# Kernel optimization log

Hardware: AMD Instinct MI355X
Metric: run time of the kernel (lower is better)

Reference implementation:

```python
import jax, jax.numpy as jnp
import numpy as np

N_NODES = 100000
N_EDGES = 1600000
IN_DIM = 128
HID = 64
CONV2_OUT = 8
GLOBAL_DIM = 24
OUT_DIM = 1
NUM_GRAPHS = 64
NEG_SLOPE = 0.01


def setup_inputs() -> dict:
    key = jax.random.key(0)
    ks = jax.random.split(key, 12)
    x = jax.random.normal(ks[0], (N_NODES, IN_DIM), dtype=jnp.float32)
    edge_index = jax.random.randint(ks[1], (2, N_EDGES), 0, N_NODES, dtype=jnp.int32)
    batch = jnp.sort(jax.random.randint(ks[2], (N_NODES,), 0, NUM_GRAPHS, dtype=jnp.int32))
    global_features = jax.random.normal(ks[3], (NUM_GRAPHS, GLOBAL_DIM), dtype=jnp.float32)
    # GCNConv weights (glorot-ish scale) and Linear weights
    W1 = jax.random.normal(ks[4], (IN_DIM, HID), dtype=jnp.float32) / np.sqrt(IN_DIM)
    b1 = jnp.zeros((HID,), dtype=jnp.float32)
    W2 = jax.random.normal(ks[5], (HID, CONV2_OUT), dtype=jnp.float32) / np.sqrt(HID)
    b2 = jnp.zeros((CONV2_OUT,), dtype=jnp.float32)
    fcW1 = jax.random.normal(ks[6], (GLOBAL_DIM + CONV2_OUT, 16), dtype=jnp.float32) / np.sqrt(GLOBAL_DIM + CONV2_OUT)
    fcb1 = jnp.zeros((16,), dtype=jnp.float32)
    fcW2 = jax.random.normal(ks[7], (16, OUT_DIM), dtype=jnp.float32) / np.sqrt(16)
    fcb2 = jnp.zeros((OUT_DIM,), dtype=jnp.float32)
    return {"x": x, "edge_index": edge_index, "batch": batch,
            "global_features": global_features,
            "W1": W1, "b1": b1, "W2": W2, "b2": b2,
            "fcW1": fcW1, "fcb1": fcb1, "fcW2": fcW2, "fcb2": fcb2}


def gcn_conv(x, src, dst, W, b):
    """PyG GCNConv: add self-loops, sym-normalize, aggregate x@W from src->dst."""
    n = x.shape[0]
    h = x @ W  # [N, F_out]
    loop = jnp.arange(n, dtype=src.dtype)
    src2 = jnp.concatenate([src, loop])
    dst2 = jnp.concatenate([dst, loop])
    deg = jax.ops.segment_sum(jnp.ones_like(dst2, dtype=h.dtype), dst2, num_segments=n)
    dinv = jnp.where(deg > 0, jax.lax.rsqrt(deg), 0.0)
    norm = dinv[src2] * dinv[dst2]  # [E+N]
    msg = h[src2] * norm[:, None]   # edge gather (dominant traffic)
    out = jax.ops.segment_sum(msg, dst2, num_segments=n)
    return out + b


def reference(x, edge_index, batch, global_features, W1, b1, W2, b2, fcW1, fcb1, fcW2, fcb2):
    src, dst = edge_index[0], edge_index[1]
    h = jax.nn.leaky_relu(gcn_conv(x, src, dst, W1, b1), NEG_SLOPE)
    h = jax.nn.leaky_relu(gcn_conv(h, src, dst, W2, b2), NEG_SLOPE)
    # global mean pool over graphs
    sums = jax.ops.segment_sum(h, batch, num_segments=NUM_GRAPHS)
    cnts = jax.ops.segment_sum(jnp.ones((h.shape[0],), h.dtype), batch, num_segments=NUM_GRAPHS)
    pool = sums / jnp.maximum(cnts, 1.0)[:, None]
    z = jnp.concatenate([pool, global_features], axis=1)
    z = jax.nn.leaky_relu(z @ fcW1 + fcb1, NEG_SLOPE)
    z = jax.nn.leaky_relu(z @ fcW2 + fcb2, NEG_SLOPE)
    return z
```

## Files before the change

### kernel.cpp

```cpp
#include <hip/hip_runtime.h>

constexpr int N_NODES = 100000;
constexpr int N_EDGES = 1600000;
constexpr int IN_DIM  = 128;
constexpr int HID     = 64;
constexpr int C2      = 8;
constexpr int GDIM    = 24;
constexpr int NG      = 64;
constexpr float SLOPE = 0.01f;
constexpr int NB_SCAN = (N_NODES + 255) / 256;

__device__ __forceinline__ float lrelu(float v) { return v > 0.f ? v : SLOPE * v; }

__device__ __forceinline__ float bflo(unsigned int u) { return __uint_as_float(u << 16); }
__device__ __forceinline__ float bfhi(unsigned int u) { return __uint_as_float(u & 0xffff0000u); }
__device__ __forceinline__ unsigned short f2bf(float f) {
    unsigned int i = __float_as_uint(f);
    unsigned int r = (i + 0x7fffu + ((i >> 16) & 1u)) >> 16;
    return (unsigned short)r;
}

__global__ void k_rank(const int* __restrict__ dst, int* __restrict__ deg,
                       int* __restrict__ rnk) {
    int t = blockIdx.x * 256 + threadIdx.x;
    if (t < N_EDGES / 4) {
        int4 d = ((const int4*)dst)[t];
        int4 r;
        r.x = atomicAdd(&deg[d.x], 1);
        r.y = atomicAdd(&deg[d.y], 1);
        r.z = atomicAdd(&deg[d.z], 1);
        r.w = atomicAdd(&deg[d.w], 1);
        ((int4*)rnk)[t] = r;
    }
}

__global__ void k_scan1(const int* __restrict__ deg, int* __restrict__ rowptr,
                        int* __restrict__ bsum, float* __restrict__ dinv) {
    __shared__ int s[256];
    int tid = threadIdx.x;
    int i = blockIdx.x * 256 + tid;
    int v = (i < N_NODES) ? deg[i] : 0;
    if (i < N_NODES) dinv[i] = rsqrtf((float)(v + 1));
    s[tid] = v;
    __syncthreads();
    for (int off = 1; off < 256; off <<= 1) {
        int t = (tid >= off) ? s[tid - off] : 0;
        __syncthreads();
        s[tid] += t;
        __syncthreads();
    }
    if (i < N_NODES) rowptr[i] = s[tid] - v;
    if (tid == 255) bsum[blockIdx.x] = s[255];
}

__global__ void k_scan2(const int* __restrict__ bsum, int* __restrict__ bsumx) {
    __shared__ int s[512];
    int tid = threadIdx.x;
    int v = (tid < NB_SCAN) ? bsum[tid] : 0;
    s[tid] = v;
    __syncthreads();
    for (int off = 1; off < 512; off <<= 1) {
        int t = (tid >= off) ? s[tid - off] : 0;
        __syncthreads();
        s[tid] += t;
        __syncthreads();
    }
    if (tid < NB_SCAN) bsumx[tid] = s[tid] - v;
}

__global__ void k_place(const int* __restrict__ src, const int* __restrict__ dst,
                        const int* __restrict__ rnk, const int* __restrict__ rowptr,
                        const int* __restrict__ bsumx, int* __restrict__ eidx) {
    int t = blockIdx.x * 256 + threadIdx.x;
    if (t < N_EDGES / 4) {
        int4 d = ((const int4*)dst)[t];
        int4 r = ((const int4*)rnk)[t];
        int4 s = ((const int4*)src)[t];
        int px = rowptr[d.x] + bsumx[d.x >> 8] + r.x;
        int py = rowptr[d.y] + bsumx[d.y >> 8] + r.y;
        int pz = rowptr[d.z] + bsumx[d.z >> 8] + r.z;
        int pw = rowptr[d.w] + bsumx[d.w >> 8] + r.w;
        eidx[px] = s.x; eidx[py] = s.y; eidx[pz] = s.z; eidx[pw] = s.w;
    }
}

__global__ __launch_bounds__(256) void k_gemm1(const float* __restrict__ x,
                                               const float* __restrict__ W1,
                                               const float* __restrict__ dinv,
                                               unsigned short* __restrict__ hs1) {
    __shared__ float sW[IN_DIM * HID];
    __shared__ float sX[32][IN_DIM];
    int node0 = blockIdx.x * 32;
    for (int t = threadIdx.x; t < IN_DIM * HID / 4; t += 256)
        ((float4*)sW)[t] = ((const float4*)W1)[t];
    for (int t = threadIdx.x; t < 32 * IN_DIM / 4; t += 256) {
        int r = t >> 5, c4 = t & 31;
        ((float4*)&sX[r][0])[c4] = ((const float4*)(x + (size_t)(node0 + r) * IN_DIM))[c4];
    }
    __syncthreads();
    int col = threadIdx.x & 63;
    int nb  = (threadIdx.x >> 6) * 8;
    float acc[8] = {0.f, 0.f, 0.f, 0.f, 0.f, 0.f, 0.f, 0.f};
    for (int k4 = 0; k4 < IN_DIM; k4 += 4) {
        float w0 = sW[(k4 + 0) * HID + col];
        float w1 = sW[(k4 + 1) * HID + col];
        float w2 = sW[(k4 + 2) * HID + col];
        float w3 = sW[(k4 + 3) * HID + col];
#pragma unroll
        for (int j = 0; j < 8; ++j) {
            float4 xv = *((const float4*)&sX[nb + j][k4]);
            acc[j] += xv.x * w0 + xv.y * w1 + xv.z * w2 + xv.w * w3;
        }
    }
#pragma unroll
    for (int j = 0; j < 8; ++j) {
        int n = node0 + nb + j;
        hs1[(size_t)n * HID + col] = f2bf(acc[j] * dinv[n]);
    }
}

__global__ __launch_bounds__(256) void k_agg1(const int* __restrict__ rowptr,
                                              const int* __restrict__ bsumx,
                                              const int* __restrict__ deg,
                                              const int* __restrict__ eidx,
                                              const unsigned short* __restrict__ hs1,
                                              const float* __restrict__ dinv,
                                              const float* __restrict__ b1,
                                              const float* __restrict__ W2,
                                              float* __restrict__ hs2) {
    int lane = threadIdx.x & 63;
    int q    = lane & 7;
    int slot = lane >> 3;
    float w2f[8];
#pragma unroll
    for (int i = 0; i < 8; ++i) w2f[i] = W2[(8 * q + i) * C2 + slot];
    float4 bb0 = ((const float4*)b1)[2 * q];
    float4 bb1 = ((const float4*)b1)[2 * q + 1];
    float bv[8] = {bb0.x, bb0.y, bb0.z, bb0.w, bb1.x, bb1.y, bb1.z, bb1.w};
    int node_base = blockIdx.x * 16 + (threadIdx.x >> 6) * 4;

    for (int nn = 0; nn < 4; ++nn) {
        int node  = node_base + nn;
        int start = rowptr[node] + bsumx[node >> 8];
        int cnt   = deg[node];
        uint4 hv = ((const uint4*)(hs1 + (size_t)node * HID))[q];
        float acc[8] = {0.f, 0.f, 0.f, 0.f, 0.f, 0.f, 0.f, 0.f};
        for (int base = 0; base < cnt; base += 64) {
            int idx = (base + lane < cnt) ? eidx[start + base + lane] : 0;
            int lim = min(64, cnt - base);
            int trips = (lim + 15) >> 4;
            for (int t = 0; t < trips; ++t) {
                int k0 = slot + t * 16;
                int k1 = k0 + 8;
                int s0 = __shfl(idx, k0);
                int s1 = __shfl(idx, k1 & 63);
                uint4 v0 = ((const uint4*)(hs1 + (size_t)s0 * HID))[q];
                uint4 v1 = ((const uint4*)(hs1 + (size_t)s1 * HID))[q];
                if (k0 >= lim) { v0.x = 0; v0.y = 0; v0.z = 0; v0.w = 0; }
                if (k1 >= lim) { v1.x = 0; v1.y = 0; v1.z = 0; v1.w = 0; }
                acc[0] += bflo(v0.x); acc[1] += bfhi(v0.x);
                acc[2] += bflo(v0.y); acc[3] += bfhi(v0.y);
                acc[4] += bflo(v0.z); acc[5] += bfhi(v0.z);
                acc[6] += bflo(v0.w); acc[7] += bfhi(v0.w);
                acc[0] += bflo(v1.x); acc[1] += bfhi(v1.x);
                acc[2] += bflo(v1.y); acc[3] += bfhi(v1.y);
                acc[4] += bflo(v1.z); acc[5] += bfhi(v1.z);
                acc[6] += bflo(v1.w); acc[7] += bfhi(v1.w);
            }
        }
#pragma unroll
        for (int m = 8; m < 64; m <<= 1)
#pragma unroll
            for (int i = 0; i < 8; ++i) acc[i] += __shfl_xor(acc[i], m);
        float self[8] = {bflo(hv.x), bfhi(hv.x), bflo(hv.y), bfhi(hv.y),
                         bflo(hv.z), bfhi(hv.z), bflo(hv.w), bfhi(hv.w)};
        float di = dinv[node];
        float p = 0.f;
#pragma unroll
        for (int i = 0; i < 8; ++i) {
            float y = lrelu(di * (acc[i] + self[i]) + bv[i]);
            p += y * w2f[i];
        }
#pragma unroll
        for (int m = 1; m < 8; m <<= 1) p += __shfl_xor(p, m);
        if (q == 0) hs2[(size_t)node * C2 + slot] = p * di;
    }
}

__global__ __launch_bounds__(256) void k_agg2(const int* __restrict__ rowptr,
                                              const int* __restrict__ bsumx,
                                              const int* __restrict__ deg,
                                              const int* __restrict__ eidx,
                                              const float* __restrict__ hs2,
                                              const float* __restrict__ dinv,
                                              const float* __restrict__ b2,
                                              float* __restrict__ y2) {
    int lane = threadIdx.x & 63;
    int q    = lane & 1;
    int slot = lane >> 1;
    int node_base = blockIdx.x * 16 + (threadIdx.x >> 6) * 4;

    for (int nn = 0; nn < 4; ++nn) {
        int node  = node_base + nn;
        int start = rowptr[node] + bsumx[node >> 8];
        int cnt   = deg[node];
        float4 acc = make_float4(0.f, 0.f, 0.f, 0.f);
        for (int base = 0; base < cnt; base += 64) {
            int idx = (base + lane < cnt) ? eidx[start + base + lane] : 0;
            int lim = min(64, cnt - base);
            int s0 = __shfl(idx, slot);
            int s1 = __shfl(idx, slot + 32);
            float4 v0 = ((const float4*)(hs2 + (size_t)s0 * C2))[q];
            float4 v1 = ((const float4*)(hs2 + (size_t)s1 * C2))[q];
            if (slot >= lim)      { v0.x = 0.f; v0.y = 0.f; v0.z = 0.f; v0.w = 0.f; }
            if (slot + 32 >= lim) { v1.x = 0.f; v1.y = 0.f; v1.z = 0.f; v1.w = 0.f; }
            acc.x += v0.x + v1.x; acc.y += v0.y + v1.y;
            acc.z += v0.z + v1.z; acc.w += v0.w + v1.w;
        }
        for (int m = 2; m < 64; m <<= 1) {
            acc.x += __shfl_xor(acc.x, m); acc.y += __shfl_xor(acc.y, m);
            acc.z += __shfl_xor(acc.z, m); acc.w += __shfl_xor(acc.w, m);
        }
        if (slot == 0) {
            float4 h = ((const float4*)(hs2 + (size_t)node * C2))[q];
            float di = dinv[node];
            const float* bb = b2 + q * 4;
            float4 r;
            r.x = lrelu(di * (acc.x + h.x) + bb[0]);
            r.y = lrelu(di * (acc.y + h.y) + bb[1]);
            r.z = lrelu(di * (acc.z + h.z) + bb[2]);
            r.w = lrelu(di * (acc.w + h.w) + bb[3]);
            ((float4*)(y2 + (size_t)node * C2))[q] = r;
        }
    }
}

__device__ __forceinline__ int lower_bound(const int* __restrict__ b, int n, int v) {
    int lo = 0, hi = n;
    while (lo < hi) {
        int m = (lo + hi) >> 1;
        if (b[m] < v) lo = m + 1; else hi = m;
    }
    return lo;
}

__global__ __launch_bounds__(256) void k_pool(const float* __restrict__ y2,
                                              const int* __restrict__ batch,
                                              const float* __restrict__ gfeat,
                                              const float* __restrict__ fcW1,
                                              const float* __restrict__ fcb1,
                                              const float* __restrict__ fcW2,
                                              const float* __restrict__ fcb2,
                                              float* __restrict__ out) {
    __shared__ float s[256];
    int g   = blockIdx.x;
    int tid = threadIdx.x;
    int start = lower_bound(batch, N_NODES, g);
    int end   = lower_bound(batch, N_NODES, g + 1);
    int col = tid & 7;
    float local = 0.f;
    for (int n = start + (tid >> 3); n < end; n += 32)
        local += y2[(size_t)n * C2 + col];
    s[tid] = local;
    __syncthreads();
    for (int off = 128; off >= 8; off >>= 1) {
        if (tid < off) s[tid] += s[tid + off];
        __syncthreads();
    }
    if (tid == 0) {
        float cnt = fmaxf((float)(end - start), 1.f);
        float z[C2 + GDIM];
        for (int c = 0; c < C2; ++c) z[c] = s[c] / cnt;
        for (int c = 0; c < GDIM; ++c) z[C2 + c] = gfeat[g * GDIM + c];
        float acc2 = fcb2[0];
        for (int j = 0; j < 16; ++j) {
            float acc = fcb1[j];
            for (int c = 0; c < C2 + GDIM; ++c) acc += z[c] * fcW1[c * 16 + j];
            acc2 += lrelu(acc) * fcW2[j];
        }
        out[g] = lrelu(acc2);
    }
}

extern "C" void kernel_launch(void* const* d_in, const int* in_sizes, int n_in,
                              void* d_out, int out_size, void* d_ws, size_t ws_size,
                              hipStream_t stream) {
    const float* x     = (const float*)d_in[0];
    const int*   ei    = (const int*)d_in[1];
    const int*   batch = (const int*)d_in[2];
    const float* gfeat = (const float*)d_in[3];
    const float* W1    = (const float*)d_in[4];
    const float* b1    = (const float*)d_in[5];
    const float* W2    = (const float*)d_in[6];
    const float* b2    = (const float*)d_in[7];
    const float* fcW1  = (const float*)d_in[8];
    const float* fcb1  = (const float*)d_in[9];
    const float* fcW2  = (const float*)d_in[10];
    const float* fcb2  = (const float*)d_in[11];
    const int* src = ei;
    const int* dst = ei + N_EDGES;

    char* ws = (char*)d_ws;
    size_t off = 0;
    auto alloc = [&](size_t bytes) -> void* {
        void* p = ws + off;
        off = (off + bytes + 255) & ~(size_t)255;
        return p;
    };
    int*   deg    = (int*)  alloc((size_t)N_NODES * 4);
    float* dinv   = (float*)alloc((size_t)N_NODES * 4);
    int*   rowptr = (int*)  alloc((size_t)N_NODES * 4);
    int*   bsum   = (int*)  alloc(512 * 4);
    int*   bsumx  = (int*)  alloc(512 * 4);
    int*   rnk    = (int*)  alloc((size_t)N_EDGES * 4);
    int*   eidx   = (int*)  alloc((size_t)N_EDGES * 4);
    unsigned short* hs1 = (unsigned short*)alloc((size_t)N_NODES * HID * 2);
    float* hs2    = (float*)alloc((size_t)N_NODES * C2 * 4);
    float* y2     = (float*)alloc((size_t)N_NODES * C2 * 4);

    hipMemsetAsync(deg, 0, (size_t)N_NODES * 4, stream);

    k_rank <<<(N_EDGES / 4 + 255) / 256, 256, 0, stream>>>(dst, deg, rnk);
    k_scan1<<<NB_SCAN, 256, 0, stream>>>(deg, rowptr, bsum, dinv);
    k_scan2<<<1, 512, 0, stream>>>(bsum, bsumx);
    k_place<<<(N_EDGES / 4 + 255) / 256, 256, 0, stream>>>(src, dst, rnk, rowptr, bsumx, eidx);

    k_gemm1<<<N_NODES / 32, 256, 0, stream>>>(x, W1, dinv, hs1);
    k_agg1 <<<N_NODES / 16, 256, 0, stream>>>(rowptr, bsumx, deg, eidx, hs1, dinv, b1, W2, hs2);
    k_agg2 <<<N_NODES / 16, 256, 0, stream>>>(rowptr, bsumx, deg, eidx, hs2, dinv, b2, y2);
    k_pool <<<NG, 256, 0, stream>>>(y2, batch, gfeat, fcW1, fcb1, fcW2, fcb2, (float*)d_out);
}
```

Before: 261.5 us.

## Replicate degree counters across blocks to reduce atomic contention in CSR build

The degree-count atomics are spread over 8 replicated counter arrays chosen by block index, which is meant to lower contention on hot destination nodes. A new kernel turns the per-replica counts into per-replica base offsets, so the placement pass needs one gathered lookup instead of the rowptr+bsumx sum. In exchange it adds an extra kernel launch, an 8x larger memset, and 8x more counter memory reads in the scan.

Result: no change. 260.8 us (-0.3%).

```diff
diff --git a/kernel.cpp b/kernel.cpp
--- a/kernel.cpp
+++ b/kernel.cpp
@@ -7,6 +7,7 @@
 constexpr int C2      = 8;
 constexpr int GDIM    = 24;
 constexpr int NG      = 64;
+constexpr int NREP    = 8;
 constexpr float SLOPE = 0.01f;
 constexpr int NB_SCAN = (N_NODES + 255) / 256;
 
@@ -20,27 +21,34 @@
     return (unsigned short)r;
 }
 
-__global__ void k_rank(const int* __restrict__ dst, int* __restrict__ deg,
+__global__ void k_rank(const int* __restrict__ dst, int* __restrict__ cnt,
                        int* __restrict__ rnk) {
     int t = blockIdx.x * 256 + threadIdx.x;
+    int* c = cnt + (size_t)(blockIdx.x & (NREP - 1)) * N_NODES;
     if (t < N_EDGES / 4) {
         int4 d = ((const int4*)dst)[t];
         int4 r;
-        r.x = atomicAdd(&deg[d.x], 1);
-        r.y = atomicAdd(&deg[d.y], 1);
-        r.z = atomicAdd(&deg[d.z], 1);
-        r.w = atomicAdd(&deg[d.w], 1);
+        r.x = atomicAdd(&c[d.x], 1);
+        r.y = atomicAdd(&c[d.y], 1);
+        r.z = atomicAdd(&c[d.z], 1);
+        r.w = atomicAdd(&c[d.w], 1);
         ((int4*)rnk)[t] = r;
     }
 }
 
-__global__ void k_scan1(const int* __restrict__ deg, int* __restrict__ rowptr,
-                        int* __restrict__ bsum, float* __restrict__ dinv) {
+__global__ void k_scan1(const int* __restrict__ cnt, int* __restrict__ deg,
+                        int* __restrict__ rowptr, int* __restrict__ bsum,
+                        float* __restrict__ dinv) {
     __shared__ int s[256];
     int tid = threadIdx.x;
     int i = blockIdx.x * 256 + tid;
-    int v = (i < N_NODES) ? deg[i] : 0;
-    if (i < N_NODES) dinv[i] = rsqrtf((float)(v + 1));
+    int v = 0;
+    if (i < N_NODES) {
+#pragma unroll
+        for (int r = 0; r < NREP; ++r) v += cnt[(size_t)r * N_NODES + i];
+        deg[i] = v;
+        dinv[i] = rsqrtf((float)(v + 1));
+    }
     s[tid] = v;
     __syncthreads();
     for (int off = 1; off < 256; off <<= 1) {
@@ -68,19 +76,33 @@
     if (tid < NB_SCAN) bsumx[tid] = s[tid] - v;
 }
 
+__global__ void k_ofs(int* __restrict__ cnt, const int* __restrict__ rowptr,
+                      const int* __restrict__ bsumx) {
+    int i = blockIdx.x * 256 + threadIdx.x;
+    if (i < N_NODES) {
+        int g = rowptr[i] + bsumx[i >> 8];
+#pragma unroll
+        for (int r = 0; r < NREP; ++r) {
+            int c = cnt[(size_t)r * N_NODES + i];
+            cnt[(size_t)r * N_NODES + i] = g;
+            g += c;
+        }
+    }
+}
+
 __global__ void k_place(const int* __restrict__ src, const int* __restrict__ dst,
-                        const int* __restrict__ rnk, const int* __restrict__ rowptr,
-                        const int* __restrict__ bsumx, int* __restrict__ eidx) {
+                        const int* __restrict__ rnk, const int* __restrict__ cnt,
+                        int* __restrict__ eidx) {
     int t = blockIdx.x * 256 + threadIdx.x;
+    const int* ofs = cnt + (size_t)(blockIdx.x & (NREP - 1)) * N_NODES;
     if (t < N_EDGES / 4) {
         int4 d = ((const int4*)dst)[t];
         int4 r = ((const int4*)rnk)[t];
         int4 s = ((const int4*)src)[t];
-        int px = rowptr[d.x] + bsumx[d.x >> 8] + r.x;
-        int py = rowptr[d.y] + bsumx[d.y >> 8] + r.y;
-        int pz = rowptr[d.z] + bsumx[d.z >> 8] + r.z;
-        int pw = rowptr[d.w] + bsumx[d.w >> 8] + r.w;
-        eidx[px] = s.x; eidx[py] = s.y; eidx[pz] = s.z; eidx[pw] = s.w;
+        eidx[ofs[d.x] + r.x] = s.x;
+        eidx[ofs[d.y] + r.y] = s.y;
+        eidx[ofs[d.z] + r.z] = s.z;
+        eidx[ofs[d.w] + r.w] = s.w;
     }
 }
 
@@ -307,6 +329,7 @@
         off = (off + bytes + 255) & ~(size_t)255;
         return p;
     };
+    int*   cnt    = (int*)  alloc((size_t)NREP * N_NODES * 4);
     int*   deg    = (int*)  alloc((size_t)N_NODES * 4);
     float* dinv   = (float*)alloc((size_t)N_NODES * 4);
     int*   rowptr = (int*)  alloc((size_t)N_NODES * 4);
@@ -318,12 +341,13 @@
     float* hs2    = (float*)alloc((size_t)N_NODES * C2 * 4);
     float* y2     = (float*)alloc((size_t)N_NODES * C2 * 4);
 
-    hipMemsetAsync(deg, 0, (size_t)N_NODES * 4, stream);
-
-    k_rank <<<(N_EDGES / 4 + 255) / 256, 256, 0, stream>>>(dst, deg, rnk);
-    k_scan1<<<NB_SCAN, 256, 0, stream>>>(deg, rowptr, bsum, dinv);
+    hipMemsetAsync(cnt, 0, (size_t)NREP * N_NODES * 4, stream);
+
+    k_rank <<<(N_EDGES / 4 + 255) / 256, 256, 0, stream>>>(dst, cnt, rnk);
+    k_scan1<<<NB_SCAN, 256, 0, stream>>>(cnt, deg, rowptr, bsum, dinv);
     k_scan2<<<1, 512, 0, stream>>>(bsum, bsumx);
-    k_place<<<(N_EDGES / 4 + 255) / 256, 256, 0, stream>>>(src, dst, rnk, rowptr, bsumx, eidx);
+    k_ofs  <<<NB_SCAN, 256, 0, stream>>>(cnt, rowptr, bsumx);
+    k_place<<<(N_EDGES / 4 + 255) / 256, 256, 0, stream>>>(src, dst, rnk, cnt, eidx);
 
     k_gemm1<<<N_NODES / 32, 256, 0, stream>>>(x, W1, dinv, hs1);
     k_agg1 <<<N_NODES / 16, 256, 0, stream>>>(rowptr, bsumx, deg, eidx, hs1, dinv, b1, W2, hs2);
```
